# Kernel optimization log

Hardware: AMD Instinct MI355X
Metric: run time of the kernel (lower is better)

The kernel has to match this reference:

```python
import jax, jax.numpy as jnp
import numpy as np

N_NODES = 100000
N_EDGES = 1000000
EDGE_F = 64
IN_C = 128
OUT_C = 256


def setup_inputs() -> dict:
    key = jax.random.key(0)
    k1, k2, k3, k4, k5, k6, k7 = jax.random.split(key, 7)
    edge_index = jax.random.randint(k1, (2, N_EDGES), 0, N_NODES, dtype=jnp.int64 if jax.config.read('jax_enable_x64') else jnp.int32)
    edge_attr = jax.random.normal(k2, (N_EDGES, EDGE_F), dtype=jnp.float32)
    node_attr = jax.random.normal(k3, (N_NODES, IN_C), dtype=jnp.float32)
    edge_weight = jax.random.uniform(k4, (N_EDGES,), dtype=jnp.float32)
    node_weight = jax.random.uniform(k5, (N_NODES,), dtype=jnp.float32)
    W = jax.random.normal(k6, (IN_C + EDGE_F, OUT_C), dtype=jnp.float32) * (1.0 / np.sqrt(IN_C + EDGE_F))
    b = jax.random.normal(k7, (OUT_C,), dtype=jnp.float32) * 0.01
    return {"edge_index": edge_index, "edge_attr": edge_attr, "node_attr": node_attr,
            "edge_weight": edge_weight, "node_weight": node_weight, "W": W, "b": b}


def reference(edge_index, edge_attr, node_attr, edge_weight, node_weight, W, b):
    num_nodes = node_attr.shape[0]
    # per-edge weighting
    ea = edge_attr * edge_weight[:, None]                       # [E, F]
    tgt = edge_index[0]                                         # [E]
    # scatter_mean over target nodes
    sums = jax.ops.segment_sum(ea, tgt, num_segments=num_nodes)                 # [N, F]
    cnt = jax.ops.segment_sum(jnp.ones_like(edge_weight), tgt, num_segments=num_nodes)  # [N]
    mean = sums / jnp.maximum(cnt, 1.0)[:, None]                # zeros for empty segments
    mean = mean * node_weight[:, None]
    x = jnp.concatenate([node_attr, mean], axis=1)              # [N, C+F]
    return jax.nn.relu(x @ W + b)                               # [N, OUT_C]
```

## Files before the change

### kernel.cpp

```cpp
#include <hip/hip_runtime.h>
#include <hip/hip_bf16.h>

#define NN 100000
#define NE 1000000
#define EF 64
#define IC 128
#define OC 256
#define NB1 391

typedef __attribute__((ext_vector_type(8))) short bf16x8;
typedef __attribute__((ext_vector_type(4))) float f32x4;

static __device__ __forceinline__ ushort f2bf(float f) {
  unsigned u = __float_as_uint(f);
  u += 0x7fffu + ((u >> 16) & 1u);
  return (ushort)(u >> 16);
}

__global__ __launch_bounds__(256) void wprep_kernel(
    const float* __restrict__ W, ushort* __restrict__ wfrag,
    int* __restrict__ cnt) {
  int t = blockIdx.x * 256 + threadIdx.x;
  int i = t & 7;
  int lane = (t >> 3) & 63;
  int ct = (t >> 9) & 15;
  int s = t >> 13;
  int k = s * 32 + (lane >> 4) * 8 + i;
  int col = ct * 16 + (lane & 15);
  wfrag[t] = f2bf(W[(size_t)k * OC + col]);
  for (int j = t; j < NN; j += 192 * 256) cnt[j] = 0;
}

__global__ __launch_bounds__(256) void hist_kernel(const int4* __restrict__ tgt4,
                                                   int* __restrict__ cnt) {
  int q = blockIdx.x * 256 + threadIdx.x;
  if (q < NE / 4) {
    int4 t = tgt4[q];
    atomicAdd(&cnt[t.x], 1);
    atomicAdd(&cnt[t.y], 1);
    atomicAdd(&cnt[t.z], 1);
    atomicAdd(&cnt[t.w], 1);
  }
}

__global__ __launch_bounds__(256) void scan1_kernel(const int* __restrict__ cnt,
                                                    int* __restrict__ bsum) {
  __shared__ int s[256];
  int t = threadIdx.x;
  int i = blockIdx.x * 256 + t;
  s[t] = (i < NN) ? cnt[i] : 0;
  __syncthreads();
  for (int off = 128; off > 0; off >>= 1) {
    if (t < off) s[t] += s[t + off];
    __syncthreads();
  }
  if (t == 0) bsum[blockIdx.x] = s[0];
}

__global__ __launch_bounds__(256) void scan23_kernel(const int* __restrict__ cnt,
                                                     const int* __restrict__ bsum,
                                                     int* __restrict__ offs,
                                                     int* __restrict__ cursor) {
  __shared__ int s[256];
  __shared__ int base_s;
  int t = threadIdx.x;
  int b = blockIdx.x;
  int part = 0;
  for (int i = t; i < b; i += 256) part += bsum[i];
  s[t] = part;
  __syncthreads();
  for (int off = 128; off > 0; off >>= 1) {
    if (t < off) s[t] += s[t + off];
    __syncthreads();
  }
  if (t == 0) base_s = s[0];
  __syncthreads();
  int base = base_s;
  int i = b * 256 + t;
  int v = (i < NN) ? cnt[i] : 0;
  s[t] = v;
  __syncthreads();
  for (int off = 1; off < 256; off <<= 1) {
    int x = (t >= off) ? s[t - off] : 0;
    __syncthreads();
    s[t] += x;
    __syncthreads();
  }
  if (i < NN) {
    int excl = s[t] - v + base;
    offs[i] = excl;
    cursor[i] = excl;
    if (i == NN - 1) offs[NN] = excl + v;
  }
}

__global__ __launch_bounds__(256) void place_kernel(const int4* __restrict__ tgt4,
                                                    const float4* __restrict__ ew4,
                                                    int* __restrict__ cursor,
                                                    int* __restrict__ eid,
                                                    float* __restrict__ ews) {
  int q = blockIdx.x * 256 + threadIdx.x;
  if (q < NE / 4) {
    int4 t = tgt4[q];
    float4 w = ew4[q];
    int e = q * 4;
    int p;
    p = atomicAdd(&cursor[t.x], 1); eid[p] = e;     ews[p] = w.x;
    p = atomicAdd(&cursor[t.y], 1); eid[p] = e + 1; ews[p] = w.y;
    p = atomicAdd(&cursor[t.z], 1); eid[p] = e + 2; ews[p] = w.z;
    p = atomicAdd(&cursor[t.w], 1); eid[p] = e + 3; ews[p] = w.w;
  }
}

__global__ __launch_bounds__(256) void agg_kernel(
    const int* __restrict__ offs, const int* __restrict__ eid,
    const float* __restrict__ ews, const float* __restrict__ ea,
    const float* __restrict__ nwt, ushort* __restrict__ mean_bf) {
  int lane = threadIdx.x & 63;
  int n = blockIdx.x * 4 + (threadIdx.x >> 6);
  if (n >= NN) return;
  int jbeg = offs[n], jend = offs[n + 1];
  int deg = jend - jbeg;
  int eg = lane >> 4;
  int fq = lane & 15;

  f32x4 acc = (f32x4)(0.0f);
  for (int j = jbeg; j < jend; j += 16) {
#pragma unroll
    for (int u = 0; u < 4; ++u) {
      int i = j + u * 4 + eg;
      int c = min(i, jend - 1);
      float w = (i < jend) ? ews[c] : 0.0f;
      int e = eid[c];
      f32x4 v = *(const f32x4*)(ea + (size_t)e * EF + fq * 4);
      acc += v * w;
    }
  }

#pragma unroll
  for (int m = 16; m <= 32; m <<= 1) {
    f32x4 o;
#pragma unroll
    for (int i = 0; i < 4; ++i) o[i] = __shfl_xor(acc[i], m, 64);
    acc += o;
  }

  if (lane < 16) {
    float scale = nwt[n] / (float)max(deg, 1);
    ushort4 o;
    o.x = f2bf(acc[0] * scale);
    o.y = f2bf(acc[1] * scale);
    o.z = f2bf(acc[2] * scale);
    o.w = f2bf(acc[3] * scale);
    *(ushort4*)(mean_bf + (size_t)n * EF + fq * 4) = o;
  }
}

__global__ __launch_bounds__(256) void gemm_kernel(
    const float* __restrict__ na, const ushort* __restrict__ mean_bf,
    const ushort* __restrict__ wfrag, const float* __restrict__ bias,
    float* __restrict__ out) {
  int tid = threadIdx.x;
  int lane = tid & 63;
  int wv = tid >> 6;
  int row_base = blockIdx.x * 64 + wv * 16;
  int r = row_base + (lane & 15);
  int rc = min(r, NN - 1);
  int kofs = (lane >> 4) * 8;
  int colb = lane & 15;

  const float* narow = na + (size_t)rc * IC;
  const ushort* mrow = mean_bf + (size_t)rc * EF;

  bf16x8 afrag[6];
#pragma unroll
  for (int s = 0; s < 4; ++s) {
    f32x4 lo = *(const f32x4*)(narow + s * 32 + kofs);
    f32x4 hi = *(const f32x4*)(narow + s * 32 + kofs + 4);
#pragma unroll
    for (int i = 0; i < 4; ++i) {
      afrag[s][i] = (short)f2bf(lo[i]);
      afrag[s][4 + i] = (short)f2bf(hi[i]);
    }
  }
#pragma unroll
  for (int s = 0; s < 2; ++s)
    afrag[4 + s] = *(const bf16x8*)(mrow + s * 32 + kofs);

  f32x4 acc[16];
#pragma unroll
  for (int ct = 0; ct < 16; ++ct) acc[ct] = (f32x4)(0.0f);

#pragma unroll
  for (int s = 0; s < 6; ++s) {
#pragma unroll
    for (int ct = 0; ct < 16; ++ct) {
      bf16x8 bfrag =
          *(const bf16x8*)(wfrag + ((size_t)((s * 16 + ct) * 64 + lane) * 8));
      acc[ct] =
          __builtin_amdgcn_mfma_f32_16x16x32_bf16(afrag[s], bfrag, acc[ct], 0, 0, 0);
    }
  }

#pragma unroll
  for (int ct = 0; ct < 16; ++ct) {
    int col = ct * 16 + colb;
    float bv = bias[col];
#pragma unroll
    for (int i = 0; i < 4; ++i) {
      int rr = row_base + (lane >> 4) * 4 + i;
      if (rr < NN) {
        float v = fmaxf(acc[ct][i] + bv, 0.0f);
        __builtin_nontemporal_store(v, out + (size_t)rr * OC + col);
      }
    }
  }
}

extern "C" void kernel_launch(void* const* d_in, const int* in_sizes, int n_in,
                              void* d_out, int out_size, void* d_ws, size_t ws_size,
                              hipStream_t stream) {
  const int* edge_index = (const int*)d_in[0];
  const float* edge_attr = (const float*)d_in[1];
  const float* node_attr = (const float*)d_in[2];
  const float* edge_weight = (const float*)d_in[3];
  const float* node_weight = (const float*)d_in[4];
  const float* W = (const float*)d_in[5];
  const float* bias = (const float*)d_in[6];
  float* out = (float*)d_out;

  char* p = (char*)d_ws;
  ushort* mean_bf = (ushort*)p;
  int* eid       = (int*)(p + 12800000);
  float* ews     = (float*)(p + 16800000);
  int* cnt       = (int*)(p + 20800000);
  int* offs      = (int*)(p + 21200000);
  int* cursor    = (int*)(p + 21600016);
  int* bsum      = (int*)(p + 22000016);
  ushort* wfrag  = (ushort*)(p + 22001600);

  wprep_kernel<<<192, 256, 0, stream>>>(W, wfrag, cnt);
  hist_kernel<<<(NE / 4 + 255) / 256, 256, 0, stream>>>((const int4*)edge_index,
                                                        cnt);
  scan1_kernel<<<NB1, 256, 0, stream>>>(cnt, bsum);
  scan23_kernel<<<NB1, 256, 0, stream>>>(cnt, bsum, offs, cursor);
  place_kernel<<<(NE / 4 + 255) / 256, 256, 0, stream>>>(
      (const int4*)edge_index, (const float4*)edge_weight, cursor, eid, ews);
  agg_kernel<<<(NN + 3) / 4, 256, 0, stream>>>(offs, eid, ews, edge_attr,
                                               node_weight, mean_bf);
  gemm_kernel<<<(NN + 63) / 64, 256, 0, stream>>>(node_attr, mean_bf, wfrag,
                                                  bias, out);
}
```

Baseline: 251.2 us.

## Merge scan kernels and stage GEMM weight fragments through double-buffered LDS

The two-pass scan is replaced by a single kernel in which each block sums all earlier counts directly. This removes a launch but makes later blocks read up to the full count array, which is quadratic-ish total traffic of about 20M reads. The GEMM now copies each 16KB slice of the bf16 weight fragments into a double-buffered shared-memory array with a __syncthreads per K-step, instead of every wave loading them from global/L2. The barriers and 32KB of LDS per block may reduce occupancy.

```diff
diff --git a/kernel.cpp b/kernel.cpp
--- a/kernel.cpp
+++ b/kernel.cpp
@@ -43,30 +43,15 @@
   }
 }
 
-__global__ __launch_bounds__(256) void scan1_kernel(const int* __restrict__ cnt,
-                                                    int* __restrict__ bsum) {
-  __shared__ int s[256];
-  int t = threadIdx.x;
-  int i = blockIdx.x * 256 + t;
-  s[t] = (i < NN) ? cnt[i] : 0;
-  __syncthreads();
-  for (int off = 128; off > 0; off >>= 1) {
-    if (t < off) s[t] += s[t + off];
-    __syncthreads();
-  }
-  if (t == 0) bsum[blockIdx.x] = s[0];
-}
-
-__global__ __launch_bounds__(256) void scan23_kernel(const int* __restrict__ cnt,
-                                                     const int* __restrict__ bsum,
-                                                     int* __restrict__ offs,
-                                                     int* __restrict__ cursor) {
+__global__ __launch_bounds__(256) void scan_kernel(const int* __restrict__ cnt,
+                                                   int* __restrict__ offs,
+                                                   int* __restrict__ cursor) {
   __shared__ int s[256];
   __shared__ int base_s;
   int t = threadIdx.x;
   int b = blockIdx.x;
   int part = 0;
-  for (int i = t; i < b; i += 256) part += bsum[i];
+  for (int i = t; i < b * 256; i += 256) part += cnt[i];
   s[t] = part;
   __syncthreads();
   for (int off = 128; off > 0; off >>= 1) {
@@ -160,6 +145,7 @@
     const float* __restrict__ na, const ushort* __restrict__ mean_bf,
     const ushort* __restrict__ wfrag, const float* __restrict__ bias,
     float* __restrict__ out) {
+  __shared__ ushort bsh[2][8192];
   int tid = threadIdx.x;
   int lane = tid & 63;
   int wv = tid >> 6;
@@ -191,12 +177,26 @@
 #pragma unroll
   for (int ct = 0; ct < 16; ++ct) acc[ct] = (f32x4)(0.0f);
 
+  {
+    const uint4* src = (const uint4*)(wfrag);
+    uint4* dst = (uint4*)bsh[0];
+#pragma unroll
+    for (int i = 0; i < 4; ++i) dst[i * 256 + tid] = src[i * 256 + tid];
+  }
+
 #pragma unroll
   for (int s = 0; s < 6; ++s) {
+    __syncthreads();
+    if (s < 5) {
+      const uint4* src = (const uint4*)(wfrag + (size_t)(s + 1) * 8192);
+      uint4* dst = (uint4*)bsh[(s + 1) & 1];
+#pragma unroll
+      for (int i = 0; i < 4; ++i) dst[i * 256 + tid] = src[i * 256 + tid];
+    }
+    const ushort* bb = bsh[s & 1];
 #pragma unroll
     for (int ct = 0; ct < 16; ++ct) {
-      bf16x8 bfrag =
-          *(const bf16x8*)(wfrag + ((size_t)((s * 16 + ct) * 64 + lane) * 8));
+      bf16x8 bfrag = *(const bf16x8*)(bb + ct * 512 + lane * 8);
       acc[ct] =
           __builtin_amdgcn_mfma_f32_16x16x32_bf16(afrag[s], bfrag, acc[ct], 0, 0, 0);
     }
@@ -236,14 +236,12 @@
   int* cnt       = (int*)(p + 20800000);
   int* offs      = (int*)(p + 21200000);
   int* cursor    = (int*)(p + 21600016);
-  int* bsum      = (int*)(p + 22000016);
-  ushort* wfrag  = (ushort*)(p + 22001600);
+  ushort* wfrag  = (ushort*)(p + 22000016);
 
   wprep_kernel<<<192, 256, 0, stream>>>(W, wfrag, cnt);
   hist_kernel<<<(NE / 4 + 255) / 256, 256, 0, stream>>>((const int4*)edge_index,
                                                         cnt);
-  scan1_kernel<<<NB1, 256, 0, stream>>>(cnt, bsum);
-  scan23_kernel<<<NB1, 256, 0, stream>>>(cnt, bsum, offs, cursor);
+  scan_kernel<<<NB1, 256, 0, stream>>>(cnt, offs, cursor);
   place_kernel<<<(NE / 4 + 255) / 256, 256, 0, stream>>>(
       (const int4*)edge_index, (const float4*)edge_weight, cursor, eid, ews);
   agg_kernel<<<(NN + 3) / 4, 256, 0, stream>>>(offs, eid, ews, edge_attr,
```

New measurement: 287.1 us. 14.3% more time.
